# Kernel tuning notes

Measured on AMD Instinct MI355X. Metric: run time of the kernel, lower is better.

## Reference

```python
import jax, jax.numpy as jnp
import numpy as np

S, B, C, H = 8192, 4, 512, 8
D = C // H
EPS = 1e-6


def setup_inputs() -> dict:
    key = jax.random.key(0)
    ks = jax.random.split(key, 11)
    scale = 1.0 / np.sqrt(C)
    return {
        "query": jax.random.normal(ks[0], (S, B, C), jnp.float32),
        "key": jax.random.normal(ks[1], (S, B, C), jnp.float32),
        "value": jax.random.normal(ks[2], (S, B, C), jnp.float32),
        "Wq": jax.random.normal(ks[3], (C, C), jnp.float32) * scale,
        "bq": jnp.zeros((C,), jnp.float32),
        "Wk": jax.random.normal(ks[4], (C, C), jnp.float32) * scale,
        "bk": jnp.zeros((C,), jnp.float32),
        "Wv": jax.random.normal(ks[5], (C, C), jnp.float32) * scale,
        "bv": jnp.zeros((C,), jnp.float32),
        "Wp": jax.random.normal(ks[6], (C, C), jnp.float32) * scale,
        "bp": jnp.zeros((C,), jnp.float32),
    }


def _elu_fm(x):
    # ELU(x) + 1 feature map
    return jax.nn.elu(x) + 1.0


def _heads(x, W, b):
    # x: [B, N, C] -> [B, H, N, D]
    y = x @ W.T + b
    Bb, N, _ = y.shape
    return y.reshape(Bb, N, H, D).transpose(0, 2, 1, 3)


def reference(query, key, value, Wq, bq, Wk, bk, Wv, bv, Wp, bp):
    # inputs [S, B, C] -> batch-first [B, S, C]
    q_in = query.transpose(1, 0, 2)
    k_in = key.transpose(1, 0, 2)
    v_in = value.transpose(1, 0, 2)

    q = _elu_fm(_heads(q_in, Wq, bq))   # [B,H,N,D]
    k = _elu_fm(_heads(k_in, Wk, bk))   # [B,H,N,D]
    v = _heads(v_in, Wv, bv)            # [B,H,N,D]

    # linear attention: O(N) kv-sum formulation
    kv = jnp.einsum('bhnd,bhnf->bhdf', k, v)       # [B,H,D,D]
    k_sum = k.sum(axis=2)                          # [B,H,D]
    qkv = jnp.einsum('bhnd,bhdf->bhnf', q, kv)     # [B,H,N,D]
    denom = jnp.einsum('bhnd,bhd->bhn', q, k_sum)  # [B,H,N]
    y = qkv / (denom[..., None] + EPS)

    # merge heads, output projection, back to [S, B, C]
    y = y.transpose(0, 2, 1, 3).reshape(q_in.shape[0], q_in.shape[1], C)
    out = y @ Wp.T + bp
    return out.transpose(1, 0, 2)
```

## Files before the change

kernel.cpp:

```cpp
#include <hip/hip_runtime.h>
#include <hip/hip_bf16.h>
#include <math.h>

#define S_LEN 8192
#define BATCH 4
#define CDIM  512
#define HEADS 8
#define DDIM  64
#define MROWS (S_LEN * BATCH)
#define EPS_F 1e-6f

typedef __attribute__((ext_vector_type(8))) short     short8_t;
typedef __attribute__((ext_vector_type(4))) float     f32x4;
typedef unsigned short ushort_t;
typedef __attribute__((ext_vector_type(8))) unsigned short ushort8_t;

static __device__ __forceinline__ ushort_t f2bf(float f) {
  __hip_bfloat16 h = __float2bfloat16(f);
  return *(ushort_t*)&h;
}

static __device__ __forceinline__ void gl2lds16(const ushort_t* g, ushort_t* l) {
  __builtin_amdgcn_global_load_lds((const __attribute__((address_space(1))) void*)g,
                                   (__attribute__((address_space(3))) void*)l,
                                   16, 0, 0);
}

#define WAIT_VM(N) asm volatile("s_waitcnt vmcnt(" #N ") lgkmcnt(0)" ::: "memory")

__global__ __launch_bounds__(256)
void cvtW_pack(const float* __restrict__ a, const float* __restrict__ b,
               const float* __restrict__ c, const float* __restrict__ d,
               ushort_t* __restrict__ oa, ushort_t* __restrict__ ob,
               ushort_t* __restrict__ oc, ushort_t* __restrict__ od) {
  const float* src = (blockIdx.y == 0) ? a : (blockIdx.y == 1) ? b :
                     (blockIdx.y == 2) ? c : d;
  ushort_t* dst    = (blockIdx.y == 0) ? oa : (blockIdx.y == 1) ? ob :
                     (blockIdx.y == 2) ? oc : od;
  const size_t i = ((size_t)blockIdx.x * 256 + threadIdx.x) * 8;
  const int n  = (int)(i >> 9);
  const int k0 = (int)(i & 511);
  const float4 x = *(const float4*)&src[i];
  const float4 y = *(const float4*)&src[i + 4];
  ushort8_t p;
  p[0] = f2bf(x.x); p[1] = f2bf(x.y); p[2] = f2bf(x.z); p[3] = f2bf(x.w);
  p[4] = f2bf(y.x); p[5] = f2bf(y.y); p[6] = f2bf(y.z); p[7] = f2bf(y.w);
  const int kf   = k0 >> 5;
  const int lane = ((k0 >> 3) & 3) * 16 + (n & 15);
  const int nfg  = n >> 4;
  *(ushort8_t*)&dst[(((size_t)nfg * 16 + kf) * 64 + lane) * 8] = p;
}

template<int AF32, int OUTF32>
static __device__ __forceinline__
void gemm128_body(const void* __restrict__ Av, const ushort_t* __restrict__ Wpk,
                  const float* __restrict__ bias, void* __restrict__ Yv,
                  const bool act, const int m0, const int n0, ushort_t* lds) {
  const int t    = threadIdx.x;
  const int w    = t >> 6;
  const int lane = t & 63;
  const int lr   = lane & 15;
  const int lk8  = (lane >> 4) * 8;
  const int wm   = (w >> 1) * 64;
  const int wn   = (w & 1) * 64;

  const float*    Xf = (const float*)Av;
  const ushort_t* Ah = (const ushort_t*)Av;

  ushort_t* Ab[2] = { lds,        lds + 4096 };
  ushort_t* Bb[2] = { lds + 8192, lds + 12288 };

  f32x4 ar[2][2][2];

  auto regloadA = [&](int set, int kt) {
    #pragma unroll
    for (int j = 0; j < 2; ++j) {
      const int fid = w * 2 + j;
      const size_t g = (size_t)(m0 + fid * 16 + lr) * CDIM + kt + lk8;
      if (set == 0) {
        ar[0][j][0] = *(const f32x4*)&Xf[g];
        ar[0][j][1] = *(const f32x4*)&Xf[g + 4];
      } else {
        ar[1][j][0] = *(const f32x4*)&Xf[g];
        ar[1][j][1] = *(const f32x4*)&Xf[g + 4];
      }
    }
  };
  auto stageA_f32 = [&](int set, ushort_t* A_) {
    #pragma unroll
    for (int j = 0; j < 2; ++j) {
      const int fid = w * 2 + j;
      const f32x4 x0 = set ? ar[1][j][0] : ar[0][j][0];
      const f32x4 x1 = set ? ar[1][j][1] : ar[0][j][1];
      short8_t v;
      v[0] = (short)f2bf(x0[0]); v[1] = (short)f2bf(x0[1]);
      v[2] = (short)f2bf(x0[2]); v[3] = (short)f2bf(x0[3]);
      v[4] = (short)f2bf(x1[0]); v[5] = (short)f2bf(x1[1]);
      v[6] = (short)f2bf(x1[2]); v[7] = (short)f2bf(x1[3]);
      *(short8_t*)&A_[(size_t)fid * 512 + lane * 8] = v;
    }
  };
  auto stageA_bf16 = [&](ushort_t* A_, int kt) {
    #pragma unroll
    for (int j = 0; j < 2; ++j) {
      const int fid = w * 2 + j;
      const ushort_t* g = Ah + (size_t)(m0 + fid * 16 + lr) * CDIM + kt + lk8;
      gl2lds16(g, &A_[fid * 512]);
    }
  };
  auto stageB = [&](ushort_t* B_, int kt) {
    #pragma unroll
    for (int j = 0; j < 2; ++j) {
      const int fid = w * 2 + j;
      const size_t idx = (size_t)((n0 >> 4) + fid) * 16 + (kt >> 5);
      gl2lds16(Wpk + idx * 512 + lane * 8, &B_[fid * 512]);
    }
  };

  f32x4 acc[4][4];
  #pragma unroll
  for (int mf = 0; mf < 4; ++mf)
    #pragma unroll
    for (int nf = 0; nf < 4; ++nf)
      acc[mf][nf] = (f32x4){0.f, 0.f, 0.f, 0.f};

  auto compute = [&](const ushort_t* A_, const ushort_t* B_) {
    short8_t afr[4], bfr[4];
    #pragma unroll
    for (int nf = 0; nf < 4; ++nf)
      bfr[nf] = *(const short8_t*)&B_[((wn >> 4) + nf) * 512 + lane * 8];
    #pragma unroll
    for (int mf = 0; mf < 4; ++mf)
      afr[mf] = *(const short8_t*)&A_[((wm >> 4) + mf) * 512 + lane * 8];
    __builtin_amdgcn_s_setprio(1);
    #pragma unroll
    for (int mf = 0; mf < 4; ++mf)
      #pragma unroll
      for (int nf = 0; nf < 4; ++nf)
        acc[mf][nf] = __builtin_amdgcn_mfma_f32_16x16x32_bf16(
            afr[mf], bfr[nf], acc[mf][nf], 0, 0, 0);
    __builtin_amdgcn_s_setprio(0);
  };

  if (AF32) {
    regloadA(0, 0);
    stageA_f32(0, Ab[0]);
    stageB(Bb[0], 0);
    regloadA(1, 32);
    regloadA(0, 64);
  } else {
    stageA_bf16(Ab[0], 0);
    stageB(Bb[0], 0);
  }
  __builtin_amdgcn_sched_barrier(0);

#define KSTEP(ks, WN)                                                      \
  do {                                                                     \
    if ((ks) <= 14) {                                                      \
      if (AF32) {                                                          \
        stageA_f32(((ks) + 1) & 1, Ab[((ks) + 1) & 1]);                    \
        stageB(Bb[((ks) + 1) & 1], ((ks) + 1) * 32);                       \
        if ((ks) <= 12) regloadA(((ks) + 1) & 1, ((ks) + 3) * 32);         \
      } else {                                                             \
        stageA_bf16(Ab[((ks) + 1) & 1], ((ks) + 1) * 32);                  \
        stageB(Bb[((ks) + 1) & 1], ((ks) + 1) * 32);                       \
      }                                                                    \
    }                                                                      \
    __builtin_amdgcn_sched_barrier(0);                                     \
    WAIT_VM(WN);                                                           \
    __builtin_amdgcn_s_barrier();                                          \
    __builtin_amdgcn_sched_barrier(0);                                     \
    compute(Ab[(ks) & 1], Bb[(ks) & 1]);                                   \
    __builtin_amdgcn_s_barrier();                                          \
  } while (0)

  if (AF32) {
    KSTEP(0, 10);  KSTEP(1, 10);  KSTEP(2, 10);  KSTEP(3, 10);
    KSTEP(4, 10);  KSTEP(5, 10);  KSTEP(6, 10);  KSTEP(7, 10);
    KSTEP(8, 10);  KSTEP(9, 10);  KSTEP(10, 10); KSTEP(11, 10);
    KSTEP(12, 10); KSTEP(13, 6);  KSTEP(14, 2);  KSTEP(15, 0);
  } else {
    KSTEP(0, 4);  KSTEP(1, 4);  KSTEP(2, 4);  KSTEP(3, 4);
    KSTEP(4, 4);  KSTEP(5, 4);  KSTEP(6, 4);  KSTEP(7, 4);
    KSTEP(8, 4);  KSTEP(9, 4);  KSTEP(10, 4); KSTEP(11, 4);
    KSTEP(12, 4); KSTEP(13, 4); KSTEP(14, 4); KSTEP(15, 0);
  }
#undef KSTEP

  if (OUTF32) {
    float* Yf = (float*)Yv;
    #pragma unroll
    for (int nf = 0; nf < 4; ++nf) {
      const int col = n0 + wn + nf * 16 + lr;
      const float bi = bias[col];
      #pragma unroll
      for (int mf = 0; mf < 4; ++mf) {
        #pragma unroll
        for (int r = 0; r < 4; ++r) {
          const int m = m0 + wm + mf * 16 + (lane >> 4) * 4 + r;
          __builtin_nontemporal_store(acc[mf][nf][r] + bi,
                                      &Yf[(size_t)m * CDIM + col]);
        }
      }
    }
  } else {
    ushort_t* Yh = (ushort_t*)Yv;
    #pragma unroll
    for (int nf = 0; nf < 4; ++nf) {
      const int col = wn + nf * 16 + lr;
      const float bi = bias[n0 + col];
      #pragma unroll
      for (int mf = 0; mf < 4; ++mf) {
        #pragma unroll
        for (int r = 0; r < 4; ++r) {
          const int row = wm + mf * 16 + (lane >> 4) * 4 + r;
          float vv = acc[mf][nf][r] + bi;
          if (act) vv = (vv > 0.f) ? (vv + 1.f) : expf(vv);
          lds[row * 128 + col] = f2bf(vv);
        }
      }
    }
    __syncthreads();
    #pragma unroll
    for (int it = 0; it < 8; ++it) {
      const int u   = it * 256 + t;
      const int row = u >> 4;
      const int c8  = (u & 15) * 8;
      const short8_t v = *(const short8_t*)&lds[u * 8];
      __builtin_nontemporal_store(
          v, (short8_t*)&Yh[(size_t)(m0 + row) * CDIM + n0 + c8]);
    }
  }
}

__global__ __launch_bounds__(256)
void proj3_128(const float* __restrict__ Xq, const float* __restrict__ Xk,
               const float* __restrict__ Xv,
               const ushort_t* __restrict__ Wqp, const ushort_t* __restrict__ Wkp,
               const ushort_t* __restrict__ Wvp,
               const float* __restrict__ bq, const float* __restrict__ bk,
               const float* __restrict__ bv,
               ushort_t* __restrict__ Yq, ushort_t* __restrict__ Yk,
               ushort_t* __restrict__ Yv) {
  __shared__ __align__(16) ushort_t lds[16384];
  const int D    = blockIdx.x;
  const int xcd  = D & 7;
  const int n    = (D >> 3) & 3;
  const int slot = D >> 5;
  const int g    = slot * 8 + xcd;
  const int m    = g & 255;
  const int z    = g >> 8;
  const float*    X    = (z == 0) ? Xq : (z == 1) ? Xk : Xv;
  const ushort_t* Wpk  = (z == 0) ? Wqp : (z == 1) ? Wkp : Wvp;
  const float*    bias = (z == 0) ? bq : (z == 1) ? bk : bv;
  ushort_t*       Y    = (z == 0) ? Yq : (z == 1) ? Yk : Yv;
  gemm128_body<1, 0>(X, Wpk, bias, Y, z < 2, m * 128, n * 128, lds);
}

__global__ __launch_bounds__(256)
void outp_128(const ushort_t* __restrict__ A, const ushort_t* __restrict__ Wpk,
              const float* __restrict__ bias, float* __restrict__ Y) {
  __shared__ __align__(16) ushort_t lds[16384];
  const int D    = blockIdx.x;
  const int xcd  = D & 7;
  const int n    = (D >> 3) & 3;
  const int slot = D >> 5;
  const int m    = slot * 8 + xcd;
  gemm128_body<0, 1>(A, Wpk, bias, Y, false, m * 128, n * 128, lds);
}

__global__ __launch_bounds__(256)
void gemm_kv(const ushort_t* __restrict__ Kb, const ushort_t* __restrict__ Vb,
             float* __restrict__ kvpart, float* __restrict__ ksumpart) {
  __shared__ __align__(16) ushort_t klds[8192];
  __shared__ __align__(16) ushort_t vlds[8192];
  const int bh    = blockIdx.x;
  const int chunk = blockIdx.y;
  const int b = bh >> 3, h = bh & 7;
  const int t = threadIdx.x;
  const int w = t >> 6;
  const int lane = t & 63;

  f32x4 acc[4];
  #pragma unroll
  for (int fg = 0; fg < 4; ++fg) acc[fg] = (f32x4){0.f, 0.f, 0.f, 0.f};
  f32x4 accs = (f32x4){0.f, 0.f, 0.f, 0.f};

  short8_t ones;
  #pragma unroll
  for (int i = 0; i < 8; ++i) ones[i] = (short)0x3F80;

  for (int round = 0; round < 4; ++round) {
    const int sbase = chunk * 512 + round * 128;
    __syncthreads();
    #pragma unroll
    for (int i = 0; i < 4; ++i) {
      const int idx  = i * 256 + t;
      const int sl   = idx >> 3;
      const int d8   = idx & 7;
      const size_t src = (size_t)((sbase + sl) * BATCH + b) * CDIM + h * DDIM + d8 * 8;
      const ushort8_t kp = *(const ushort8_t*)&Kb[src];
      const ushort8_t vp = *(const ushort8_t*)&Vb[src];
      const int sb  = sl >> 5;
      const int j   = sl & 7;
      const int lp0 = (d8 & 1) * 8 + ((sl >> 3) & 3) * 16;
      const int dg  = d8 >> 1;
      const int kbase = ((sb * 4 + dg) * 64 + lp0) * 8 + j;
      #pragma unroll
      for (int e = 0; e < 8; ++e) {
        klds[kbase + e * 8] = kp[e];
        vlds[kbase + e * 8] = vp[e];
      }
    }
    __syncthreads();
    #pragma unroll
    for (int sb = 0; sb < 4; ++sb) {
      const short8_t af = *(const short8_t*)&klds[((sb * 4 + w) * 64 + lane) * 8];
      accs = __builtin_amdgcn_mfma_f32_16x16x32_bf16(af, ones, accs, 0, 0, 0);
      #pragma unroll
      for (int fg = 0; fg < 4; ++fg) {
        const short8_t bf = *(const short8_t*)&vlds[((sb * 4 + fg) * 64 + lane) * 8];
        acc[fg] = __builtin_amdgcn_mfma_f32_16x16x32_bf16(af, bf, acc[fg], 0, 0, 0);
      }
    }
  }

  const size_t obase = ((size_t)bh * 16 + chunk) * 64;
  #pragma unroll
  for (int fg = 0; fg < 4; ++fg)
    #pragma unroll
    for (int r = 0; r < 4; ++r) {
      const int d = w * 16 + (lane >> 4) * 4 + r;
      kvpart[(obase + d) * 64 + fg * 16 + (lane & 15)] = acc[fg][r];
    }
  if ((lane & 15) == 0) {
    #pragma unroll
    for (int r = 0; r < 4; ++r)
      ksumpart[obase + w * 16 + (lane >> 4) * 4 + r] = accs[r];
  }
}

__global__ __launch_bounds__(256)
void kv_finish(const float* __restrict__ kvpart, const float* __restrict__ ksumpart,
               ushort_t* __restrict__ kvT) {
  const int bh = blockIdx.x;
  const int t  = threadIdx.x;
  for (int idx = t; idx < 4096; idx += 256) {
    const int d = idx >> 6, f = idx & 63;
    float s = 0.f;
    for (int c = 0; c < 16; ++c)
      s += kvpart[(((size_t)bh * 16 + c) * 64 + d) * 64 + f];
    kvT[((size_t)bh * 80 + f) * 64 + d] = f2bf(s);
  }
  if (t < 64) {
    float s = 0.f;
    for (int c = 0; c < 16; ++c)
      s += ksumpart[((size_t)bh * 16 + c) * 64 + t];
    kvT[((size_t)bh * 80 + 64) * 64 + t] = f2bf(s);
  }
  for (int i = t; i < 15 * 64; i += 256)
    kvT[((size_t)bh * 80 + 65) * 64 + i] = 0;
}

__global__ __launch_bounds__(256)
void gemm_qkv(ushort_t* __restrict__ Qb, const ushort_t* __restrict__ kvT) {
  __shared__ __align__(16) ushort_t alds[8192];
  __shared__ __align__(16) ushort_t blds[5120];
  const int bh    = blockIdx.x;
  const int chunk = blockIdx.y;
  const int b = bh >> 3, h = bh & 7;
  const int t = threadIdx.x;
  const int w = t >> 6;
  const int lane = t & 63;
  const int lr = lane & 15;
  const int lk = (lane >> 4) * 8;

  #pragma unroll
  for (int i = 0; i < 4; ++i) {
    const int fidx = w * 4 + i;
    const int ks = fidx >> 3, fm = fidx & 7;
    const ushort_t* src = Qb +
        (size_t)((chunk * 128 + fm * 16 + lr) * BATCH + b) * CDIM +
        h * DDIM + ks * 32 + lk;
    gl2lds16(src, &alds[fidx * 512]);
  }
  for (int idx = w; idx < 10; idx += 4) {
    const int ks = idx / 5, fg = idx % 5;
    const ushort_t* src = kvT + (size_t)(bh * 80 + fg * 16 + lr) * 64 + ks * 32 + lk;
    gl2lds16(src, &blds[idx * 512]);
  }
  __syncthreads();

  f32x4 acc[2][5];
  #pragma unroll
  for (int mi = 0; mi < 2; ++mi)
    #pragma unroll
    for (int fg = 0; fg < 5; ++fg)
      acc[mi][fg] = (f32x4){0.f, 0.f, 0.f, 0.f};

  #pragma unroll
  for (int ks = 0; ks < 2; ++ks) {
    short8_t af[2], bf[5];
    #pragma unroll
    for (int mi = 0; mi < 2; ++mi)
      af[mi] = *(const short8_t*)&alds[(ks * 8 + w * 2 + mi) * 512 + lane * 8];
    #pragma unroll
    for (int fg = 0; fg < 5; ++fg)
      bf[fg] = *(const short8_t*)&blds[(ks * 5 + fg) * 512 + lane * 8];
    #pragma unroll
    for (int mi = 0; mi < 2; ++mi)
      #pragma unroll
      for (int fg = 0; fg < 5; ++fg)
        acc[mi][fg] = __builtin_amdgcn_mfma_f32_16x16x32_bf16(
            af[mi], bf[fg], acc[mi][fg], 0, 0, 0);
  }

  #pragma unroll
  for (int mi = 0; mi < 2; ++mi) {
    #pragma unroll
    for (int r = 0; r < 4; ++r) {
      const float dv  = __shfl(acc[mi][4][r], lane & 48);
      const float inv = 1.f / (dv + EPS_F);
      const int s = chunk * 128 + w * 32 + mi * 16 + (lane >> 4) * 4 + r;
      const size_t rowb = (size_t)(s * BATCH + b) * CDIM + h * DDIM;
      #pragma unroll
      for (int fg = 0; fg < 4; ++fg)
        Qb[rowb + fg * 16 + lr] = f2bf(acc[mi][fg][r] * inv);
    }
  }
}

extern "C" void kernel_launch(void* const* d_in, const int* in_sizes, int n_in,
                              void* d_out, int out_size, void* d_ws, size_t ws_size,
                              hipStream_t stream) {
  const float* q_in = (const float*)d_in[0];
  const float* k_in = (const float*)d_in[1];
  const float* v_in = (const float*)d_in[2];
  const float* Wq   = (const float*)d_in[3];
  const float* bq   = (const float*)d_in[4];
  const float* Wk   = (const float*)d_in[5];
  const float* bk   = (const float*)d_in[6];
  const float* Wv   = (const float*)d_in[7];
  const float* bv   = (const float*)d_in[8];
  const float* Wp   = (const float*)d_in[9];
  const float* bp   = (const float*)d_in[10];
  float* out = (float*)d_out;

  const size_t NTOK = (size_t)MROWS * CDIM;
  const size_t NW   = (size_t)CDIM * CDIM;
  ushort_t* Wqp    = (ushort_t*)d_ws;
  ushort_t* Wkp    = Wqp + NW;
  ushort_t* Wvp    = Wkp + NW;
  ushort_t* Wpp    = Wvp + NW;
  ushort_t* qbuf   = Wpp + NW;
  ushort_t* kbuf   = qbuf + NTOK;
  ushort_t* vbuf   = kbuf + NTOK;
  ushort_t* kvT    = vbuf + NTOK;
  float* kvpart    = (float*)(kvT + (size_t)32 * 80 * 64);
  float* ksumpart  = kvpart + (size_t)512 * 64 * 64;

  const dim3 blk(256);

  cvtW_pack<<<dim3(128, 4), blk, 0, stream>>>(Wq, Wk, Wv, Wp,
                                              Wqp, Wkp, Wvp, Wpp);

  proj3_128<<<dim3(3072), blk, 0, stream>>>(
      q_in, k_in, v_in, Wqp, Wkp, Wvp, bq, bk, bv, qbuf, kbuf, vbuf);

  gemm_kv<<<dim3(32, 16), blk, 0, stream>>>(kbuf, vbuf, kvpart, ksumpart);
  kv_finish<<<dim3(32), blk, 0, stream>>>(kvpart, ksumpart, kvT);

  gemm_qkv<<<dim3(32, 64), blk, 0, stream>>>(qbuf, kvT);

  outp_128<<<dim3(1024), blk, 0, stream>>>(qbuf, Wpp, bp, out);
}
```

Measured before the change: 209.1 us.

## Stage fp32 activations directly into LDS via async loads, convert at fragment read

```diff
diff --git a/kernel.cpp b/kernel.cpp
--- a/kernel.cpp
+++ b/kernel.cpp
@@ -20,7 +20,16 @@
   return *(ushort_t*)&h;
 }
 
-static __device__ __forceinline__ void gl2lds16(const ushort_t* g, ushort_t* l) {
+static __device__ __forceinline__ short8_t cvt8(f32x4 lo, f32x4 hi) {
+  short8_t v;
+  v[0] = (short)f2bf(lo[0]); v[1] = (short)f2bf(lo[1]);
+  v[2] = (short)f2bf(lo[2]); v[3] = (short)f2bf(lo[3]);
+  v[4] = (short)f2bf(hi[0]); v[5] = (short)f2bf(hi[1]);
+  v[6] = (short)f2bf(hi[2]); v[7] = (short)f2bf(hi[3]);
+  return v;
+}
+
+static __device__ __forceinline__ void gl2lds16(const void* g, void* l) {
   __builtin_amdgcn_global_load_lds((const __attribute__((address_space(1))) void*)g,
                                    (__attribute__((address_space(3))) void*)l,
                                    16, 0, 0);
@@ -67,37 +76,20 @@
   const float*    Xf = (const float*)Av;
   const ushort_t* Ah = (const ushort_t*)Av;
 
-  ushort_t* Ab[2] = { lds,        lds + 4096 };
-  ushort_t* Bb[2] = { lds + 8192, lds + 12288 };
-
-  f32x4 ar[2][2][2];
-
-  auto regloadA = [&](int set, int kt) {
+  const int ABUFU = AF32 ? 8192 : 4096;
+  ushort_t* Ab[2] = { lds, lds + ABUFU };
+  ushort_t* Bb[2] = { lds + 2 * ABUFU, lds + 2 * ABUFU + 4096 };
+
+  auto stageA_f32 = [&](ushort_t* A_, int kt) {
     #pragma unroll
     for (int j = 0; j < 2; ++j) {
       const int fid = w * 2 + j;
-      const size_t g = (size_t)(m0 + fid * 16 + lr) * CDIM + kt + lk8;
-      if (set == 0) {
-        ar[0][j][0] = *(const f32x4*)&Xf[g];
-        ar[0][j][1] = *(const f32x4*)&Xf[g + 4];
-      } else {
-        ar[1][j][0] = *(const f32x4*)&Xf[g];
-        ar[1][j][1] = *(const f32x4*)&Xf[g + 4];
-      }
-    }
-  };
-  auto stageA_f32 = [&](int set, ushort_t* A_) {
-    #pragma unroll
-    for (int j = 0; j < 2; ++j) {
-      const int fid = w * 2 + j;
-      const f32x4 x0 = set ? ar[1][j][0] : ar[0][j][0];
-      const f32x4 x1 = set ? ar[1][j][1] : ar[0][j][1];
-      short8_t v;
-      v[0] = (short)f2bf(x0[0]); v[1] = (short)f2bf(x0[1]);
-      v[2] = (short)f2bf(x0[2]); v[3] = (short)f2bf(x0[3]);
-      v[4] = (short)f2bf(x1[0]); v[5] = (short)f2bf(x1[1]);
-      v[6] = (short)f2bf(x1[2]); v[7] = (short)f2bf(x1[3]);
-      *(short8_t*)&A_[(size_t)fid * 512 + lane * 8] = v;
+      #pragma unroll
+      for (int h = 0; h < 2; ++h) {
+        const float* g = Xf + (size_t)(m0 + fid * 16 + lr) * CDIM +
+                         kt + lk8 + h * 4;
+        gl2lds16(g, &A_[(fid * 2 + h) * 512]);
+      }
     }
   };
   auto stageA_bf16 = [&](ushort_t* A_, int kt) {
@@ -129,9 +121,20 @@
     #pragma unroll
     for (int nf = 0; nf < 4; ++nf)
       bfr[nf] = *(const short8_t*)&B_[((wn >> 4) + nf) * 512 + lane * 8];
-    #pragma unroll
-    for (int mf = 0; mf < 4; ++mf)
-      afr[mf] = *(const short8_t*)&A_[((wm >> 4) + mf) * 512 + lane * 8];
+    if (AF32) {
+      const float* Afl = (const float*)A_;
+      #pragma unroll
+      for (int mf = 0; mf < 4; ++mf) {
+        const int fid = (wm >> 4) + mf;
+        const f32x4 lo = *(const f32x4*)&Afl[((fid * 2 + 0) * 64 + lane) * 4];
+        const f32x4 hi = *(const f32x4*)&Afl[((fid * 2 + 1) * 64 + lane) * 4];
+        afr[mf] = cvt8(lo, hi);
+      }
+    } else {
+      #pragma unroll
+      for (int mf = 0; mf < 4; ++mf)
+        afr[mf] = *(const short8_t*)&A_[((wm >> 4) + mf) * 512 + lane * 8];
+    }
     __builtin_amdgcn_s_setprio(1);
     #pragma unroll
     for (int mf = 0; mf < 4; ++mf)
@@ -142,29 +145,16 @@
     __builtin_amdgcn_s_setprio(0);
   };
 
-  if (AF32) {
-    regloadA(0, 0);
-    stageA_f32(0, Ab[0]);
-    stageB(Bb[0], 0);
-    regloadA(1, 32);
-    regloadA(0, 64);
-  } else {
-    stageA_bf16(Ab[0], 0);
-    stageB(Bb[0], 0);
-  }
+  if (AF32) stageA_f32(Ab[0], 0); else stageA_bf16(Ab[0], 0);
+  stageB(Bb[0], 0);
   __builtin_amdgcn_sched_barrier(0);
 
 #define KSTEP(ks, WN)                                                      \
   do {                                                                     \
     if ((ks) <= 14) {                                                      \
-      if (AF32) {                                                          \
-        stageA_f32(((ks) + 1) & 1, Ab[((ks) + 1) & 1]);                    \
-        stageB(Bb[((ks) + 1) & 1], ((ks) + 1) * 32);                       \
-        if ((ks) <= 12) regloadA(((ks) + 1) & 1, ((ks) + 3) * 32);         \
-      } else {                                                             \
-        stageA_bf16(Ab[((ks) + 1) & 1], ((ks) + 1) * 32);                  \
-        stageB(Bb[((ks) + 1) & 1], ((ks) + 1) * 32);                       \
-      }                                                                    \
+      if (AF32) stageA_f32(Ab[((ks) + 1) & 1], ((ks) + 1) * 32);           \
+      else      stageA_bf16(Ab[((ks) + 1) & 1], ((ks) + 1) * 32);          \
+      stageB(Bb[((ks) + 1) & 1], ((ks) + 1) * 32);                         \
     }                                                                      \
     __builtin_amdgcn_sched_barrier(0);                                     \
     WAIT_VM(WN);                                                           \
@@ -175,10 +165,10 @@
   } while (0)
 
   if (AF32) {
-    KSTEP(0, 10);  KSTEP(1, 10);  KSTEP(2, 10);  KSTEP(3, 10);
-    KSTEP(4, 10);  KSTEP(5, 10);  KSTEP(6, 10);  KSTEP(7, 10);
-    KSTEP(8, 10);  KSTEP(9, 10);  KSTEP(10, 10); KSTEP(11, 10);
-    KSTEP(12, 10); KSTEP(13, 6);  KSTEP(14, 2);  KSTEP(15, 0);
+    KSTEP(0, 6);  KSTEP(1, 6);  KSTEP(2, 6);  KSTEP(3, 6);
+    KSTEP(4, 6);  KSTEP(5, 6);  KSTEP(6, 6);  KSTEP(7, 6);
+    KSTEP(8, 6);  KSTEP(9, 6);  KSTEP(10, 6); KSTEP(11, 6);
+    KSTEP(12, 6); KSTEP(13, 6); KSTEP(14, 6); KSTEP(15, 0);
   } else {
     KSTEP(0, 4);  KSTEP(1, 4);  KSTEP(2, 4);  KSTEP(3, 4);
     KSTEP(4, 4);  KSTEP(5, 4);  KSTEP(6, 4);  KSTEP(7, 4);
@@ -242,7 +232,7 @@
                const float* __restrict__ bv,
                ushort_t* __restrict__ Yq, ushort_t* __restrict__ Yk,
                ushort_t* __restrict__ Yv) {
-  __shared__ __align__(16) ushort_t lds[16384];
+  __shared__ __align__(16) ushort_t lds[24576];
   const int D    = blockIdx.x;
   const int xcd  = D & 7;
   const int n    = (D >> 3) & 3;
```

Result: faster. 203.0 us, median of 2 (-2.9%).

## Triple-buffer LDS stages in projection GEMMs for deeper prefetch

Applied to the files above, without the earlier changes.

```diff
diff --git a/kernel.cpp b/kernel.cpp
--- a/kernel.cpp
+++ b/kernel.cpp
@@ -20,7 +20,7 @@
   return *(ushort_t*)&h;
 }
 
-static __device__ __forceinline__ void gl2lds16(const ushort_t* g, ushort_t* l) {
+static __device__ __forceinline__ void gl2lds16(const void* g, void* l) {
   __builtin_amdgcn_global_load_lds((const __attribute__((address_space(1))) void*)g,
                                    (__attribute__((address_space(3))) void*)l,
                                    16, 0, 0);
@@ -67,8 +67,8 @@
   const float*    Xf = (const float*)Av;
   const ushort_t* Ah = (const ushort_t*)Av;
 
-  ushort_t* Ab[2] = { lds,        lds + 4096 };
-  ushort_t* Bb[2] = { lds + 8192, lds + 12288 };
+  ushort_t* Ab[3] = { lds, lds + 4096, lds + 8192 };
+  ushort_t* Bb[3] = { lds + 12288, lds + 16384, lds + 20480 };
 
   f32x4 ar[2][2][2];
 
@@ -86,7 +86,7 @@
       }
     }
   };
-  auto stageA_f32 = [&](int set, ushort_t* A_) {
+  auto stageA_cvt = [&](int set, ushort_t* A_) {
     #pragma unroll
     for (int j = 0; j < 2; ++j) {
       const int fid = w * 2 + j;
@@ -100,7 +100,7 @@
       *(short8_t*)&A_[(size_t)fid * 512 + lane * 8] = v;
     }
   };
-  auto stageA_bf16 = [&](ushort_t* A_, int kt) {
+  auto stageA_dma = [&](ushort_t* A_, int kt) {
     #pragma unroll
     for (int j = 0; j < 2; ++j) {
       const int fid = w * 2 + j;
@@ -144,46 +144,45 @@
 
   if (AF32) {
     regloadA(0, 0);
-    stageA_f32(0, Ab[0]);
-    stageB(Bb[0], 0);
     regloadA(1, 32);
-    regloadA(0, 64);
+    stageA_cvt(0, Ab[0]); stageB(Bb[0], 0);  regloadA(0, 64);
+    stageA_cvt(1, Ab[1]); stageB(Bb[1], 32); regloadA(1, 96);
   } else {
-    stageA_bf16(Ab[0], 0);
-    stageB(Bb[0], 0);
+    stageA_dma(Ab[0], 0);  stageB(Bb[0], 0);
+    stageA_dma(Ab[1], 32); stageB(Bb[1], 32);
   }
   __builtin_amdgcn_sched_barrier(0);
 
 #define KSTEP(ks, WN)                                                      \
   do {                                                                     \
-    if ((ks) <= 14) {                                                      \
+    if ((ks) <= 13) {                                                      \
       if (AF32) {                                                          \
-        stageA_f32(((ks) + 1) & 1, Ab[((ks) + 1) & 1]);                    \
-        stageB(Bb[((ks) + 1) & 1], ((ks) + 1) * 32);                       \
-        if ((ks) <= 12) regloadA(((ks) + 1) & 1, ((ks) + 3) * 32);         \
+        stageA_cvt((ks) & 1, Ab[((ks) + 2) % 3]);                          \
+        stageB(Bb[((ks) + 2) % 3], ((ks) + 2) * 32);                       \
+        if ((ks) <= 11) regloadA((ks) & 1, ((ks) + 4) * 32);               \
       } else {                                                             \
-        stageA_bf16(Ab[((ks) + 1) & 1], ((ks) + 1) * 32);                  \
-        stageB(Bb[((ks) + 1) & 1], ((ks) + 1) * 32);                       \
+        stageA_dma(Ab[((ks) + 2) % 3], ((ks) + 2) * 32);                   \
+        stageB(Bb[((ks) + 2) % 3], ((ks) + 2) * 32);                       \
       }                                                                    \
     }                                                                      \
     __builtin_amdgcn_sched_barrier(0);                                     \
     WAIT_VM(WN);                                                           \
     __builtin_amdgcn_s_barrier();                                          \
     __builtin_amdgcn_sched_barrier(0);                                     \
-    compute(Ab[(ks) & 1], Bb[(ks) & 1]);                                   \
+    compute(Ab[(ks) % 3], Bb[(ks) % 3]);                                   \
     __builtin_amdgcn_s_barrier();                                          \
   } while (0)
 
   if (AF32) {
-    KSTEP(0, 10);  KSTEP(1, 10);  KSTEP(2, 10);  KSTEP(3, 10);
-    KSTEP(4, 10);  KSTEP(5, 10);  KSTEP(6, 10);  KSTEP(7, 10);
-    KSTEP(8, 10);  KSTEP(9, 10);  KSTEP(10, 10); KSTEP(11, 10);
-    KSTEP(12, 10); KSTEP(13, 6);  KSTEP(14, 2);  KSTEP(15, 0);
+    KSTEP(0, 12);  KSTEP(1, 12);  KSTEP(2, 12);  KSTEP(3, 12);
+    KSTEP(4, 12);  KSTEP(5, 12);  KSTEP(6, 12);  KSTEP(7, 12);
+    KSTEP(8, 12);  KSTEP(9, 12);  KSTEP(10, 12); KSTEP(11, 12);
+    KSTEP(12, 12); KSTEP(13, 8);  KSTEP(14, 2);  KSTEP(15, 0);
   } else {
-    KSTEP(0, 4);  KSTEP(1, 4);  KSTEP(2, 4);  KSTEP(3, 4);
-    KSTEP(4, 4);  KSTEP(5, 4);  KSTEP(6, 4);  KSTEP(7, 4);
-    KSTEP(8, 4);  KSTEP(9, 4);  KSTEP(10, 4); KSTEP(11, 4);
-    KSTEP(12, 4); KSTEP(13, 4); KSTEP(14, 4); KSTEP(15, 0);
+    KSTEP(0, 8);  KSTEP(1, 8);  KSTEP(2, 8);  KSTEP(3, 8);
+    KSTEP(4, 8);  KSTEP(5, 8);  KSTEP(6, 8);  KSTEP(7, 8);
+    KSTEP(8, 8);  KSTEP(9, 8);  KSTEP(10, 8); KSTEP(11, 8);
+    KSTEP(12, 8); KSTEP(13, 8); KSTEP(14, 4); KSTEP(15, 0);
   }
 #undef KSTEP
 
@@ -242,7 +241,7 @@
                const float* __restrict__ bv,
                ushort_t* __restrict__ Yq, ushort_t* __restrict__ Yk,
                ushort_t* __restrict__ Yv) {
-  __shared__ __align__(16) ushort_t lds[16384];
+  __shared__ __align__(16) ushort_t lds[24576];
   const int D    = blockIdx.x;
   const int xcd  = D & 7;
   const int n    = (D >> 3) & 3;
@@ -260,7 +259,7 @@
 __global__ __launch_bounds__(256)
 void outp_128(const ushort_t* __restrict__ A, const ushort_t* __restrict__ Wpk,
               const float* __restrict__ bias, float* __restrict__ Y) {
-  __shared__ __align__(16) ushort_t lds[16384];
+  __shared__ __align__(16) ushort_t lds[24576];
   const int D    = blockIdx.x;
   const int xcd  = D & 7;
   const int n    = (D >> 3) & 3;
```

Result: slower. 225.9 us (+8.0%).
